# Performance work log

Measured on AMD Instinct MI355X. Metric: run time of the kernel, lower is better.

Reference implementation:

```python
import jax, jax.numpy as jnp
import numpy as np

T, H, I, E, K = 4096, 1024, 2048, 32, 4


def setup_inputs() -> dict:
    key = jax.random.key(0)
    ks = jax.random.split(key, 8)
    s = lambda k, shape, std: (jax.random.normal(k, shape, jnp.float32) * std)
    return {
        "x": s(ks[0], (T, H), 1.0),
        "router_w": s(ks[1], (E, H), 0.02),
        "gate_w": s(ks[2], (E, H, I), 0.02),
        "up_w": s(ks[3], (E, H, I), 0.02),
        "down_w": s(ks[4], (E, I, H), 0.02),
        "shared_gate_w": s(ks[5], (H, I), 0.02),
        "shared_up_w": s(ks[6], (H, I), 0.02),
        "shared_down_w": s(ks[7], (I, H), 0.02),
        "top_k": K,
    }


def _moe_forward(x, router_w, gate_w, up_w, down_w, sg, su, sd, top_k):
    # x: [T, H]; expert weights: gate/up [E, H, I], down [E, I, H]
    Tn = x.shape[0]
    En = router_w.shape[0]

    # Router: softmax over experts, top-k selection, renormalize selected probs
    logits = x @ router_w.T                                   # [T, E]
    probs = jax.nn.softmax(logits, axis=-1)
    topk_p, topk_i = jax.lax.top_k(probs, top_k)              # [T, K]
    topk_p = topk_p / jnp.sum(topk_p, axis=-1, keepdims=True)

    # Dense combine weights: combine[t, e] = routing weight of expert e for token t
    combine = jnp.zeros((Tn, En), x.dtype).at[
        jnp.arange(Tn)[:, None], topk_i].add(topk_p)          # [T, E]

    def expert_step(acc, inp):
        wg, wu, wd, c = inp                                   # [H,I], [H,I], [I,H], [T]
        h = jax.nn.silu(x @ wg) * (x @ wu)                    # [T, I] SwiGLU
        return acc + c[:, None] * (h @ wd), None

    acc0 = jnp.zeros_like(x)
    out, _ = jax.lax.scan(expert_step, acc0,
                          (gate_w, up_w, down_w, combine.T))

    # Shared expert: always applied
    shared = (jax.nn.silu(x @ sg) * (x @ su)) @ sd            # [T, H]
    return out + shared


def reference(x, router_w, gate_w, up_w, down_w,
              shared_gate_w, shared_up_w, shared_down_w, top_k):
    return _moe_forward(x, router_w, gate_w, up_w, down_w,
                        shared_gate_w, shared_up_w, shared_down_w, top_k)
```

## Files before the change

kernel.cpp:

```cpp
#include <hip/hip_runtime.h>
#include <hip/hip_bf16.h>

#define T_TOK 4096
#define H_DIM 1024
#define I_DIM 2048
#define N_EXP 32
#define TOPK  4
#define TKTOT (T_TOK * TOPK)
#define ROWS_MAX 24576
#define MAX_TILES 192
#define BM 128
#define BK 64
#define LDB 72

typedef _Float16 f16;
typedef __attribute__((ext_vector_type(2))) f16  f16x2;
typedef __attribute__((ext_vector_type(4))) f16  f16x4;
typedef __attribute__((ext_vector_type(8))) f16  f16x8;
typedef __attribute__((ext_vector_type(4))) float f32x4;

__device__ __forceinline__ void glds16(const f16* g, f16* l) {
  __builtin_amdgcn_global_load_lds(
      (const __attribute__((address_space(1))) void*)g,
      (__attribute__((address_space(3))) void*)l, 16, 0, 0);
}
__device__ __forceinline__ void sfence() { __builtin_amdgcn_sched_barrier(0); }
__device__ __forceinline__ void bar_vm36() {
  sfence();
  asm volatile("s_waitcnt vmcnt(36) lgkmcnt(0)" ::: "memory");
  sfence();
  __builtin_amdgcn_s_barrier();
  sfence();
}
__device__ __forceinline__ void bar_vm20() {
  sfence();
  asm volatile("s_waitcnt vmcnt(20) lgkmcnt(0)" ::: "memory");
  sfence();
  __builtin_amdgcn_s_barrier();
  sfence();
}
__device__ __forceinline__ void bar_vm12() {
  sfence();
  asm volatile("s_waitcnt vmcnt(12) lgkmcnt(0)" ::: "memory");
  sfence();
  __builtin_amdgcn_s_barrier();
  sfence();
}
__device__ __forceinline__ void bar_vm0() {
  sfence();
  asm volatile("s_waitcnt vmcnt(0) lgkmcnt(0)" ::: "memory");
  sfence();
  __builtin_amdgcn_s_barrier();
  sfence();
}
__device__ __forceinline__ void bar_post() {
  sfence();
  __builtin_amdgcn_s_barrier();
  sfence();
}

__global__ void prep_kernel(const float* __restrict__ x, f16* __restrict__ xb,
                            int* __restrict__ row_token,
                            int* __restrict__ counts) {
  int gid = blockIdx.x * blockDim.x + threadIdx.x;
  float4 v = *(const float4*)(x + (size_t)gid * 4);
  f16x4 hv = { (f16)v.x, (f16)v.y, (f16)v.z, (f16)v.w };
  *(f16x4*)(xb + (size_t)gid * 4) = hv;
  if (gid < ROWS_MAX) row_token[gid] = (gid < T_TOK) ? gid : 0;
  if (gid < N_EXP) counts[gid] = 0;
}

__global__ void router_kernel(const float* __restrict__ x,
                              const float* __restrict__ rw,
                              int* __restrict__ expert_sel,
                              float* __restrict__ weight_sel,
                              int* __restrict__ counts) {
  int wid = threadIdx.x >> 6, lane = threadIdx.x & 63;
  int t = blockIdx.x * 4 + wid;
  float xr[16];
#pragma unroll
  for (int j = 0; j < 16; ++j) xr[j] = x[(size_t)t * H_DIM + lane + j * 64];
  float l[32];
#pragma unroll
  for (int e = 0; e < 32; ++e) {
    float p = 0.f;
#pragma unroll
    for (int j = 0; j < 16; ++j) p += xr[j] * rw[(size_t)e * H_DIM + lane + j * 64];
#pragma unroll
    for (int off = 32; off; off >>= 1) p += __shfl_xor(p, off, 64);
    l[e] = p;
  }
  if (lane == 0) {
    unsigned used = 0;
    int sel[4]; float lv[4];
#pragma unroll
    for (int k = 0; k < 4; ++k) {
      float bv = -3.4e38f; int bi = 0;
#pragma unroll
      for (int e = 0; e < 32; ++e) {
        bool better = (((used >> e) & 1u) == 0u) && (l[e] > bv);
        bv = better ? l[e] : bv;
        bi = better ? e : bi;
      }
      used |= 1u << bi; sel[k] = bi; lv[k] = bv;
    }
    float m = lv[0];
    float p0 = __expf(lv[0] - m), p1 = __expf(lv[1] - m);
    float p2 = __expf(lv[2] - m), p3 = __expf(lv[3] - m);
    float s = p0 + p1 + p2 + p3;
    float wv[4] = { p0 / s, p1 / s, p2 / s, p3 / s };
#pragma unroll
    for (int k = 0; k < 4; ++k) {
      expert_sel[t * 4 + k] = sel[k];
      weight_sel[t * 4 + k] = wv[k];
      atomicAdd(&counts[sel[k]], 1);
    }
  }
}

__global__ void scan_kernel(const int* __restrict__ counts, int* __restrict__ cursor,
                            int* __restrict__ tile_expert, int* __restrict__ tile_row0,
                            int* __restrict__ ntiles) {
  if (threadIdx.x != 0 || blockIdx.x != 0) return;
  int nt = 0;
  for (int i = 0; i < T_TOK / BM; ++i) { tile_expert[nt] = N_EXP; tile_row0[nt] = i * BM; ++nt; }
  int pos = T_TOK;
  for (int e = 0; e < N_EXP; ++e) {
    cursor[e] = pos;
    int c = counts[e];
    int nte = (c + BM - 1) / BM;
    for (int i = 0; i < nte; ++i) { tile_expert[nt] = e; tile_row0[nt] = pos + i * BM; ++nt; }
    pos += nte * BM;
  }
  ntiles[0] = nt;
}

__global__ void scatter_kernel(const int* __restrict__ expert_sel,
                               int* __restrict__ cursor,
                               int* __restrict__ row_token,
                               int* __restrict__ slot_of) {
  int i = blockIdx.x * blockDim.x + threadIdx.x;
  if (i >= TKTOT) return;
  int e = expert_sel[i];
  int pos = atomicAdd(&cursor[e], 1);
  row_token[pos] = i >> 2;
  slot_of[i] = pos;
}

struct Bf2 { float2 g[8]; };
__device__ __forceinline__ Bf2 fetch_b2(const float* __restrict__ src, size_t ldn) {
  Bf2 r;
#pragma unroll
  for (int j = 0; j < 8; ++j) r.g[j] = *(const float2*)(src + (size_t)j * ldn);
  return r;
}
__device__ __forceinline__ void write_b2(const Bf2& b,
                                         f16 (*__restrict__ Bs)[LDB], int nq, int kr) {
  const float* ga = (const float*)b.g;
  int ks = (8 * kr) ^ ((nq & 7) << 3);
#pragma unroll
  for (int i = 0; i < 2; ++i) {
    union { f16x2 p[4]; f16x8 v; } u;
#pragma unroll
    for (int j = 0; j < 4; ++j)
      u.p[j] = __builtin_bit_cast(
          f16x2, __builtin_amdgcn_cvt_pkrtz(ga[(2 * j) * 2 + i],
                                            ga[(2 * j + 1) * 2 + i]));
    *(f16x8*)&Bs[2 * nq + i][ks] = u.v;
  }
}
__device__ __forceinline__ int rswz1(int row, int kf16) {
  return kf16 ^ (((row >> 1) & 7) << 3);
}

struct Bf4 { float4 g[8]; };
__device__ __forceinline__ Bf4 fetch_b4(const float* __restrict__ src, size_t ldn) {
  Bf4 r;
#pragma unroll
  for (int j = 0; j < 8; ++j) r.g[j] = *(const float4*)(src + (size_t)j * ldn);
  return r;
}
__device__ __forceinline__ void write_b4(const Bf4& b,
                                         f16 (*__restrict__ Bs)[LDB], int nq, int kr) {
  const float* ga = (const float*)b.g;
  int ks = (8 * kr) ^ ((nq & 7) << 3);
#pragma unroll
  for (int i = 0; i < 4; ++i) {
    union { f16x2 p[4]; f16x8 v; } u;
#pragma unroll
    for (int j = 0; j < 4; ++j)
      u.p[j] = __builtin_bit_cast(
          f16x2, __builtin_amdgcn_cvt_pkrtz(ga[(2 * j) * 4 + i],
                                            ga[(2 * j + 1) * 4 + i]));
    *(f16x8*)&Bs[4 * nq + i][ks] = u.v;
  }
}
__device__ __forceinline__ int rswz2(int row, int kf16) {
  return kf16 ^ (((row >> 2) & 7) << 3);
}

__global__ __launch_bounds__(256, 2) void gemm1_kernel(
    const f16* __restrict__ xb,
    const float* __restrict__ gate_w, const float* __restrict__ up_w,
    const float* __restrict__ sgw, const float* __restrict__ suw,
    const int* __restrict__ row_token,
    const int* __restrict__ tile_expert, const int* __restrict__ tile_row0,
    const int* __restrict__ ntiles, f16* __restrict__ hbuf) {
  int d = blockIdx.y * gridDim.x + blockIdx.x;
  int l = (d & 7) * 768 + (d >> 3);
  int bx = l % MAX_TILES;
  int n0 = (l / MAX_TILES) * 64;
  if (bx >= ntiles[0]) return;
  int e = tile_expert[bx];
  int row0 = tile_row0[bx];
  const float* wg = (e < N_EXP) ? gate_w + (size_t)e * H_DIM * I_DIM : sgw;
  const float* wu = (e < N_EXP) ? up_w   + (size_t)e * H_DIM * I_DIM : suw;

  __shared__ __align__(16) f16 smem[2 * BM * BK + 2 * 64 * LDB];
  f16* A0 = smem;
  f16* A1 = smem + BM * BK;
  f16 (*Bg)[LDB] = (f16(*)[LDB])(smem + 2 * BM * BK);
  f16 (*Bu)[LDB] = (f16(*)[LDB])(smem + 2 * BM * BK + 64 * LDB);
  f16 (*Ct)[LDB] = (f16(*)[LDB])smem;

  int tid = threadIdx.x;
  int lane = tid & 63, wid = tid >> 6;
  int wm = wid >> 1, wn = wid & 1;
  int lr = lane & 15, lk = (lane >> 4) * 8;
  int nq = tid & 31, kr = tid >> 5;

  const f16* abase[4];
#pragma unroll
  for (int it = 0; it < 4; ++it) {
    int idx = tid + it * 256;
    int arow = idx >> 3;
    int atok = row_token[row0 + arow];
    abase[it] = xb + (size_t)atok * H_DIM + ((((idx & 7)) ^ (arow & 7)) << 3);
  }
  const float* wgp = wg + (size_t)(8 * kr) * I_DIM + n0 + 2 * nq;
  const float* wup = wu + (size_t)(8 * kr) * I_DIM + n0 + 2 * nq;

  f32x4 accg[4][2], accu[4][2];
#pragma unroll
  for (int m = 0; m < 4; ++m)
#pragma unroll
    for (int n = 0; n < 2; ++n) { accg[m][n] = (f32x4)0.f; accu[m][n] = (f32x4)0.f; }

  const int NK = H_DIM / BK;

  sfence();
#pragma unroll
  for (int it = 0; it < 4; ++it)
    glds16(abase[it], A0 + (tid + it * 256) * 8);
  sfence();
  Bf2 g0 = fetch_b2(wgp, I_DIM);
  Bf2 u0 = fetch_b2(wup, I_DIM);
  sfence();
  Bf2 g1 = fetch_b2(wgp + (size_t)BK * I_DIM, I_DIM);
  Bf2 u1 = fetch_b2(wup + (size_t)BK * I_DIM, I_DIM);
  sfence();

#define G1_MFMA(ASRC)                                                        \
  {                                                                          \
    const f16* As_ = (ASRC);                                                 \
    __builtin_amdgcn_s_setprio(1);                                           \
    _Pragma("unroll")                                                        \
    for (int kk = 0; kk < BK; kk += 32) {                                    \
      f16x8 a[4], bg[2], bu[2];                                              \
      _Pragma("unroll")                                                      \
      for (int m = 0; m < 4; ++m) {                                          \
        int ar = wm * 64 + m * 16 + lr;                                      \
        int ko = (kk + lk) ^ ((ar & 7) << 3);                                \
        a[m] = *(const f16x8*)(As_ + ar * BK + ko);                          \
      }                                                                      \
      _Pragma("unroll")                                                      \
      for (int n = 0; n < 2; ++n) {                                          \
        int rowb = wn * 32 + n * 16 + lr;                                    \
        int ko = rswz1(rowb, kk + lk);                                       \
        bg[n] = *(const f16x8*)&Bg[rowb][ko];                                \
        bu[n] = *(const f16x8*)&Bu[rowb][ko];                                \
      }                                                                      \
      _Pragma("unroll")                                                      \
      for (int m = 0; m < 4; ++m)                                            \
        _Pragma("unroll")                                                    \
        for (int n = 0; n < 2; ++n) {                                        \
          accg[m][n] = __builtin_amdgcn_mfma_f32_16x16x32_f16(a[m], bg[n], accg[m][n], 0, 0, 0); \
          accu[m][n] = __builtin_amdgcn_mfma_f32_16x16x32_f16(a[m], bu[n], accu[m][n], 0, 0, 0); \
        }                                                                    \
    }                                                                        \
    __builtin_amdgcn_s_setprio(0);                                           \
  }

  for (int ks = 0; ks < NK - 2; ks += 2) {
    {
      write_b2(g0, Bg, nq, kr);
      write_b2(u0, Bu, nq, kr);
      sfence();
#pragma unroll
      for (int it = 0; it < 4; ++it)
        glds16(abase[it] + (ks + 1) * BK, A1 + (tid + it * 256) * 8);
      sfence();
      g0 = fetch_b2(wgp + (size_t)(ks + 2) * BK * I_DIM, I_DIM);
      u0 = fetch_b2(wup + (size_t)(ks + 2) * BK * I_DIM, I_DIM);
      sfence();
      bar_vm36();
      G1_MFMA(A0);
      bar_post();
    }
    {
      write_b2(g1, Bg, nq, kr);
      write_b2(u1, Bu, nq, kr);
      sfence();
#pragma unroll
      for (int it = 0; it < 4; ++it)
        glds16(abase[it] + (ks + 2) * BK, A0 + (tid + it * 256) * 8);
      sfence();
      g1 = fetch_b2(wgp + (size_t)(ks + 3) * BK * I_DIM, I_DIM);
      u1 = fetch_b2(wup + (size_t)(ks + 3) * BK * I_DIM, I_DIM);
      sfence();
      bar_vm36();
      G1_MFMA(A1);
      bar_post();
    }
  }
  {
    write_b2(g0, Bg, nq, kr);
    write_b2(u0, Bu, nq, kr);
    sfence();
#pragma unroll
    for (int it = 0; it < 4; ++it)
      glds16(abase[it] + (NK - 1) * BK, A1 + (tid + it * 256) * 8);
    sfence();
    bar_vm20();
    G1_MFMA(A0);
    bar_post();
  }
  {
    write_b2(g1, Bg, nq, kr);
    write_b2(u1, Bu, nq, kr);
    bar_vm0();
    G1_MFMA(A1);
  }
#undef G1_MFMA

  __syncthreads();
#pragma unroll
  for (int m = 0; m < 4; ++m)
#pragma unroll
    for (int n = 0; n < 2; ++n)
#pragma unroll
      for (int j = 0; j < 4; ++j) {
        float g = accg[m][n][j], u = accu[m][n][j];
        float hv = g / (1.f + __expf(-g)) * u;
        Ct[wm * 64 + m * 16 + (lane >> 4) * 4 + j][wn * 32 + n * 16 + lr] = (f16)hv;
      }
  __syncthreads();
#pragma unroll
  for (int it = 0; it < 4; ++it) {
    int idx = tid + it * 256;
    int r = idx >> 3, g8 = (idx & 7) * 8;
    *(f16x8*)(hbuf + (size_t)(row0 + r) * I_DIM + n0 + g8) = *(const f16x8*)&Ct[r][g8];
  }
}

__global__ __launch_bounds__(256, 2) void gemm2_kernel(
    const f16* __restrict__ hbuf,
    const float* __restrict__ down_w, const float* __restrict__ sdw,
    const int* __restrict__ tile_expert, const int* __restrict__ tile_row0,
    const int* __restrict__ ntiles, f16* __restrict__ ybuf) {
  int d = blockIdx.y * gridDim.x + blockIdx.x;
  int l = (d & 7) * 192 + (d >> 3);
  int bx = l % MAX_TILES;
  int n0 = (l / MAX_TILES) * 128;
  if (bx >= ntiles[0]) return;
  int e = tile_expert[bx];
  int row0 = tile_row0[bx];
  const float* wd = (e < N_EXP) ? down_w + (size_t)e * I_DIM * H_DIM : sdw;

  __shared__ __align__(16) f16 smem[2 * BM * BK + 128 * LDB];
  f16* A0 = smem;
  f16* A1 = smem + BM * BK;
  f16 (*Bd)[LDB] = (f16(*)[LDB])(smem + 2 * BM * BK);
  f16 (*Ct)[136] = (f16(*)[136])smem;

  int tid = threadIdx.x;
  int lane = tid & 63, wid = tid >> 6;
  int wm = wid >> 1, wn = wid & 1;
  int lr = lane & 15, lk = (lane >> 4) * 8;
  int nq = tid & 31, kr = tid >> 5;

  const f16* abase[4];
#pragma unroll
  for (int it = 0; it < 4; ++it) {
    int idx = tid + it * 256;
    int arow = idx >> 3;
    abase[it] = hbuf + (size_t)(row0 + arow) * I_DIM + ((((idx & 7)) ^ (arow & 7)) << 3);
  }
  const float* wdp = wd + (size_t)(8 * kr) * H_DIM + n0 + 4 * nq;

  f32x4 acc[4][4];
#pragma unroll
  for (int m = 0; m < 4; ++m)
#pragma unroll
    for (int n = 0; n < 4; ++n) acc[m][n] = (f32x4)0.f;

  const int NK = I_DIM / BK;

  sfence();
#pragma unroll
  for (int it = 0; it < 4; ++it)
    glds16(abase[it], A0 + (tid + it * 256) * 8);
  sfence();
  Bf4 d0 = fetch_b4(wdp, H_DIM);
  sfence();
  Bf4 d1 = fetch_b4(wdp + (size_t)BK * H_DIM, H_DIM);
  sfence();

#define G2_MFMA(ASRC)                                                        \
  {                                                                          \
    const f16* As_ = (ASRC);                                                 \
    __builtin_amdgcn_s_setprio(1);                                           \
    _Pragma("unroll")                                                        \
    for (int kk = 0; kk < BK; kk += 32) {                                    \
      f16x8 a[4], bd[4];                                                     \
      _Pragma("unroll")                                                      \
      for (int m = 0; m < 4; ++m) {                                          \
        int ar = wm * 64 + m * 16 + lr;                                      \
        int ko = (kk + lk) ^ ((ar & 7) << 3);                                \
        a[m] = *(const f16x8*)(As_ + ar * BK + ko);                          \
      }                                                                      \
      _Pragma("unroll")                                                      \
      for (int n = 0; n < 4; ++n) {                                          \
        int rowb = wn * 64 + n * 16 + lr;                                    \
        bd[n] = *(const f16x8*)&Bd[rowb][rswz2(rowb, kk + lk)];              \
      }                                                                      \
      _Pragma("unroll")                                                      \
      for (int m = 0; m < 4; ++m)                                            \
        _Pragma("unroll")                                                    \
        for (int n = 0; n < 4; ++n)                                          \
          acc[m][n] = __builtin_amdgcn_mfma_f32_16x16x32_f16(a[m], bd[n], acc[m][n], 0, 0, 0); \
    }                                                                        \
    __builtin_amdgcn_s_setprio(0);                                           \
  }

  for (int ks = 0; ks < NK - 2; ks += 2) {
    {
      write_b4(d0, Bd, nq, kr);
      sfence();
#pragma unroll
      for (int it = 0; it < 4; ++it)
        glds16(abase[it] + (ks + 1) * BK, A1 + (tid + it * 256) * 8);
      sfence();
      d0 = fetch_b4(wdp + (size_t)(ks + 2) * BK * H_DIM, H_DIM);
      sfence();
      bar_vm20();
      G2_MFMA(A0);
      bar_post();
    }
    {
      write_b4(d1, Bd, nq, kr);
      sfence();
#pragma unroll
      for (int it = 0; it < 4; ++it)
        glds16(abase[it] + (ks + 2) * BK, A0 + (tid + it * 256) * 8);
      sfence();
      d1 = fetch_b4(wdp + (size_t)(ks + 3) * BK * H_DIM, H_DIM);
      sfence();
      bar_vm20();
      G2_MFMA(A1);
      bar_post();
    }
  }
  {
    write_b4(d0, Bd, nq, kr);
    sfence();
#pragma unroll
    for (int it = 0; it < 4; ++it)
      glds16(abase[it] + (NK - 1) * BK, A1 + (tid + it * 256) * 8);
    sfence();
    bar_vm12();
    G2_MFMA(A0);
    bar_post();
  }
  {
    write_b4(d1, Bd, nq, kr);
    bar_vm0();
    G2_MFMA(A1);
  }
#undef G2_MFMA

  __syncthreads();
#pragma unroll
  for (int m = 0; m < 4; ++m)
#pragma unroll
    for (int n = 0; n < 4; ++n)
#pragma unroll
      for (int j = 0; j < 4; ++j)
        Ct[wm * 64 + m * 16 + (lane >> 4) * 4 + j][wn * 64 + n * 16 + lr] =
            (f16)acc[m][n][j];
  __syncthreads();
#pragma unroll
  for (int it = 0; it < 8; ++it) {
    int idx = tid + it * 256;
    int r = idx >> 4, g8 = (idx & 15) * 8;
    *(f16x8*)(ybuf + (size_t)(row0 + r) * H_DIM + n0 + g8) = *(const f16x8*)&Ct[r][g8];
  }
}

__global__ void gather_kernel(const f16* __restrict__ ybuf,
                              const int* __restrict__ slot_of,
                              const float* __restrict__ weight_sel,
                              float* __restrict__ out) {
  int gid = blockIdx.x * blockDim.x + threadIdx.x;
  int t = gid >> 7, s8 = (gid & 127) * 8;
  f16x8 ysh = *(const f16x8*)(ybuf + (size_t)t * H_DIM + s8);
  float a[8];
#pragma unroll
  for (int j = 0; j < 8; ++j) a[j] = (float)ysh[j];
#pragma unroll
  for (int k = 0; k < 4; ++k) {
    int sl = slot_of[t * 4 + k];
    float w = weight_sel[t * 4 + k];
    f16x8 v = *(const f16x8*)(ybuf + (size_t)sl * H_DIM + s8);
#pragma unroll
    for (int j = 0; j < 8; ++j) a[j] += w * (float)v[j];
  }
  float4 o0 = { a[0], a[1], a[2], a[3] };
  float4 o1 = { a[4], a[5], a[6], a[7] };
  *(float4*)(out + (size_t)t * H_DIM + s8) = o0;
  *(float4*)(out + (size_t)t * H_DIM + s8 + 4) = o1;
}

extern "C" void kernel_launch(void* const* d_in, const int* in_sizes, int n_in,
                              void* d_out, int out_size, void* d_ws, size_t ws_size,
                              hipStream_t stream) {
  const float* x        = (const float*)d_in[0];
  const float* router_w = (const float*)d_in[1];
  const float* gate_w   = (const float*)d_in[2];
  const float* up_w     = (const float*)d_in[3];
  const float* down_w   = (const float*)d_in[4];
  const float* sgw      = (const float*)d_in[5];
  const float* suw      = (const float*)d_in[6];
  const float* sdw      = (const float*)d_in[7];
  float* out = (float*)d_out;

  char* w = (char*)d_ws;
  f16*   xb         = (f16*)w;   w += (size_t)T_TOK * H_DIM * 2;
  int*   expert_sel = (int*)w;   w += (size_t)TKTOT * 4;
  float* weight_sel = (float*)w; w += (size_t)TKTOT * 4;
  int*   slot_of    = (int*)w;   w += (size_t)TKTOT * 4;
  int*   counts     = (int*)w;   w += 256;
  int*   cursor     = (int*)w;   w += 256;
  int*   tile_exp   = (int*)w;   w += MAX_TILES * 4;
  int*   tile_row0  = (int*)w;   w += MAX_TILES * 4;
  int*   ntiles     = (int*)w;   w += 256;
  int*   row_token  = (int*)w;   w += (size_t)ROWS_MAX * 4;
  f16*   hbuf       = (f16*)w;   w += (size_t)ROWS_MAX * I_DIM * 2;
  f16*   ybuf       = (f16*)w;   w += (size_t)ROWS_MAX * H_DIM * 2;
  if ((size_t)(w - (char*)d_ws) > ws_size) return;

  prep_kernel<<<(T_TOK * H_DIM / 4) / 256, 256, 0, stream>>>(x, xb, row_token, counts);
  router_kernel<<<T_TOK / 4, 256, 0, stream>>>(x, router_w, expert_sel, weight_sel, counts);
  scan_kernel<<<1, 64, 0, stream>>>(counts, cursor, tile_exp, tile_row0, ntiles);
  scatter_kernel<<<TKTOT / 256, 256, 0, stream>>>(expert_sel, cursor, row_token, slot_of);
  gemm1_kernel<<<dim3(MAX_TILES, I_DIM / 64), 256, 0, stream>>>(
      xb, gate_w, up_w, sgw, suw, row_token, tile_exp, tile_row0, ntiles, hbuf);
  gemm2_kernel<<<dim3(MAX_TILES, H_DIM / 128), 256, 0, stream>>>(
      hbuf, down_w, sdw, tile_exp, tile_row0, ntiles, ybuf);
  gather_kernel<<<(T_TOK * (H_DIM / 8)) / 256, 256, 0, stream>>>(
      ybuf, slot_of, weight_sel, out);
}
```

Baseline: 678.7 us.

## Split gate/up GEMMs across 8-warp blocks, double-buffer B tiles, parallelize tile scan

Both grouped GEMM kernels now launch 512 threads per block instead of 256. In gemm1, warps 0-3 compute the gate projection and warps 4-7 the up projection, and SiLU and the product are applied in the epilogue through shared memory. gemm2 spreads its 128-column tile over 8 warps, and both kernels double-buffer the B tile in LDS with adjusted vmcnt waits. The tile-building scan becomes a wavefront shuffle prefix sum instead of a single-thread loop. This lowers per-thread register and accumulator pressure and adds latency hiding, at the cost of doubled B staging LDS and an f16 rounding step before the gate*up multiply.

After: 676.1 us. No clear change (-0.4%).

```diff
diff --git a/kernel.cpp b/kernel.cpp
--- a/kernel.cpp
+++ b/kernel.cpp
@@ -25,23 +25,16 @@
       (__attribute__((address_space(3))) void*)l, 16, 0, 0);
 }
 __device__ __forceinline__ void sfence() { __builtin_amdgcn_sched_barrier(0); }
-__device__ __forceinline__ void bar_vm36() {
-  sfence();
-  asm volatile("s_waitcnt vmcnt(36) lgkmcnt(0)" ::: "memory");
+__device__ __forceinline__ void bar_vm18() {
+  sfence();
+  asm volatile("s_waitcnt vmcnt(18) lgkmcnt(0)" ::: "memory");
   sfence();
   __builtin_amdgcn_s_barrier();
   sfence();
 }
-__device__ __forceinline__ void bar_vm20() {
-  sfence();
-  asm volatile("s_waitcnt vmcnt(20) lgkmcnt(0)" ::: "memory");
-  sfence();
-  __builtin_amdgcn_s_barrier();
-  sfence();
-}
-__device__ __forceinline__ void bar_vm12() {
-  sfence();
-  asm volatile("s_waitcnt vmcnt(12) lgkmcnt(0)" ::: "memory");
+__device__ __forceinline__ void bar_vm10() {
+  sfence();
+  asm volatile("s_waitcnt vmcnt(10) lgkmcnt(0)" ::: "memory");
   sfence();
   __builtin_amdgcn_s_barrier();
   sfence();
@@ -121,18 +114,32 @@
 __global__ void scan_kernel(const int* __restrict__ counts, int* __restrict__ cursor,
                             int* __restrict__ tile_expert, int* __restrict__ tile_row0,
                             int* __restrict__ ntiles) {
-  if (threadIdx.x != 0 || blockIdx.x != 0) return;
-  int nt = 0;
-  for (int i = 0; i < T_TOK / BM; ++i) { tile_expert[nt] = N_EXP; tile_row0[nt] = i * BM; ++nt; }
-  int pos = T_TOK;
-  for (int e = 0; e < N_EXP; ++e) {
-    cursor[e] = pos;
-    int c = counts[e];
-    int nte = (c + BM - 1) / BM;
-    for (int i = 0; i < nte; ++i) { tile_expert[nt] = e; tile_row0[nt] = pos + i * BM; ++nt; }
-    pos += nte * BM;
-  }
-  ntiles[0] = nt;
+  int lane = threadIdx.x;
+  if (lane < T_TOK / BM) { tile_expert[lane] = N_EXP; tile_row0[lane] = lane * BM; }
+  int nte = 0, rows = 0;
+  if (lane < N_EXP) {
+    int c = counts[lane];
+    nte = (c + BM - 1) / BM;
+    rows = nte * BM;
+  }
+  int pnte = nte, prows = rows;
+#pragma unroll
+  for (int off = 1; off < 64; off <<= 1) {
+    int t1 = __shfl_up(pnte, off, 64);
+    int t2 = __shfl_up(prows, off, 64);
+    if (lane >= off) { pnte += t1; prows += t2; }
+  }
+  int excl_nte = pnte - nte, excl_rows = prows - rows;
+  if (lane < N_EXP) {
+    int pos = T_TOK + excl_rows;
+    cursor[lane] = pos;
+    int tb = T_TOK / BM + excl_nte;
+    for (int i = 0; i < nte; ++i) {
+      tile_expert[tb + i] = lane;
+      tile_row0[tb + i] = pos + i * BM;
+    }
+    if (lane == N_EXP - 1) ntiles[0] = tb + nte;
+  }
 }
 
 __global__ void scatter_kernel(const int* __restrict__ expert_sel,
@@ -154,8 +161,8 @@
   for (int j = 0; j < 8; ++j) r.g[j] = *(const float2*)(src + (size_t)j * ldn);
   return r;
 }
-__device__ __forceinline__ void write_b2(const Bf2& b,
-                                         f16 (*__restrict__ Bs)[LDB], int nq, int kr) {
+__device__ __forceinline__ void write_b2(const Bf2& b, f16* __restrict__ Bs,
+                                         int nq, int kr) {
   const float* ga = (const float*)b.g;
   int ks = (8 * kr) ^ ((nq & 7) << 3);
 #pragma unroll
@@ -166,40 +173,14 @@
       u.p[j] = __builtin_bit_cast(
           f16x2, __builtin_amdgcn_cvt_pkrtz(ga[(2 * j) * 2 + i],
                                             ga[(2 * j + 1) * 2 + i]));
-    *(f16x8*)&Bs[2 * nq + i][ks] = u.v;
+    *(f16x8*)(Bs + (2 * nq + i) * LDB + ks) = u.v;
   }
 }
 __device__ __forceinline__ int rswz1(int row, int kf16) {
   return kf16 ^ (((row >> 1) & 7) << 3);
 }
 
-struct Bf4 { float4 g[8]; };
-__device__ __forceinline__ Bf4 fetch_b4(const float* __restrict__ src, size_t ldn) {
-  Bf4 r;
-#pragma unroll
-  for (int j = 0; j < 8; ++j) r.g[j] = *(const float4*)(src + (size_t)j * ldn);
-  return r;
-}
-__device__ __forceinline__ void write_b4(const Bf4& b,
-                                         f16 (*__restrict__ Bs)[LDB], int nq, int kr) {
-  const float* ga = (const float*)b.g;
-  int ks = (8 * kr) ^ ((nq & 7) << 3);
-#pragma unroll
-  for (int i = 0; i < 4; ++i) {
-    union { f16x2 p[4]; f16x8 v; } u;
-#pragma unroll
-    for (int j = 0; j < 4; ++j)
-      u.p[j] = __builtin_bit_cast(
-          f16x2, __builtin_amdgcn_cvt_pkrtz(ga[(2 * j) * 4 + i],
-                                            ga[(2 * j + 1) * 4 + i]));
-    *(f16x8*)&Bs[4 * nq + i][ks] = u.v;
-  }
-}
-__device__ __forceinline__ int rswz2(int row, int kf16) {
-  return kf16 ^ (((row >> 2) & 7) << 3);
-}
-
-__global__ __launch_bounds__(256, 2) void gemm1_kernel(
+__global__ __launch_bounds__(512, 2) void gemm1_kernel(
     const f16* __restrict__ xb,
     const float* __restrict__ gate_w, const float* __restrict__ up_w,
     const float* __restrict__ sgw, const float* __restrict__ suw,
@@ -216,57 +197,59 @@
   const float* wg = (e < N_EXP) ? gate_w + (size_t)e * H_DIM * I_DIM : sgw;
   const float* wu = (e < N_EXP) ? up_w   + (size_t)e * H_DIM * I_DIM : suw;
 
-  __shared__ __align__(16) f16 smem[2 * BM * BK + 2 * 64 * LDB];
+  __shared__ __align__(16) f16 smem[2 * BM * BK + 2 * 2 * 64 * LDB];
   f16* A0 = smem;
   f16* A1 = smem + BM * BK;
-  f16 (*Bg)[LDB] = (f16(*)[LDB])(smem + 2 * BM * BK);
-  f16 (*Bu)[LDB] = (f16(*)[LDB])(smem + 2 * BM * BK + 64 * LDB);
-  f16 (*Ct)[LDB] = (f16(*)[LDB])smem;
+  f16* Bbase = smem + 2 * BM * BK;
+  f16* Ctg = Bbase;
+  f16* Ctu = Bbase + 9216;
 
   int tid = threadIdx.x;
   int lane = tid & 63, wid = tid >> 6;
-  int wm = wid >> 1, wn = wid & 1;
+  int mat = wid >> 2;
+  int w4 = wid & 3;
+  int wm = w4 >> 1, wn = w4 & 1;
   int lr = lane & 15, lk = (lane >> 4) * 8;
-  int nq = tid & 31, kr = tid >> 5;
-
-  const f16* abase[4];
-#pragma unroll
-  for (int it = 0; it < 4; ++it) {
-    int idx = tid + it * 256;
-    int arow = idx >> 3;
-    int atok = row_token[row0 + arow];
-    abase[it] = xb + (size_t)atok * H_DIM + ((((idx & 7)) ^ (arow & 7)) << 3);
-  }
-  const float* wgp = wg + (size_t)(8 * kr) * I_DIM + n0 + 2 * nq;
-  const float* wup = wu + (size_t)(8 * kr) * I_DIM + n0 + 2 * nq;
-
-  f32x4 accg[4][2], accu[4][2];
+
+  int t8 = tid & 255;
+  int nq = t8 & 31, kr = t8 >> 5;
+  const float* wsrc = (mat ? wu : wg) + (size_t)(8 * kr) * I_DIM + n0 + 2 * nq;
+
+  const f16* abase0;
+  const f16* abase1;
+  {
+    int idx = tid;
+    int arow = idx >> 3, sl = idx & 7;
+    abase0 = xb + (size_t)row_token[row0 + arow] * H_DIM + ((sl ^ (arow & 7)) << 3);
+    idx = tid + 512;
+    arow = idx >> 3; sl = idx & 7;
+    abase1 = xb + (size_t)row_token[row0 + arow] * H_DIM + ((sl ^ (arow & 7)) << 3);
+  }
+
+  f32x4 acc[4][2];
 #pragma unroll
   for (int m = 0; m < 4; ++m)
 #pragma unroll
-    for (int n = 0; n < 2; ++n) { accg[m][n] = (f32x4)0.f; accu[m][n] = (f32x4)0.f; }
+    for (int n = 0; n < 2; ++n) acc[m][n] = (f32x4)0.f;
 
   const int NK = H_DIM / BK;
 
-  sfence();
-#pragma unroll
-  for (int it = 0; it < 4; ++it)
-    glds16(abase[it], A0 + (tid + it * 256) * 8);
-  sfence();
-  Bf2 g0 = fetch_b2(wgp, I_DIM);
-  Bf2 u0 = fetch_b2(wup, I_DIM);
-  sfence();
-  Bf2 g1 = fetch_b2(wgp + (size_t)BK * I_DIM, I_DIM);
-  Bf2 u1 = fetch_b2(wup + (size_t)BK * I_DIM, I_DIM);
-  sfence();
-
-#define G1_MFMA(ASRC)                                                        \
+  Bf2 pb0 = fetch_b2(wsrc, I_DIM);
+  sfence();
+  glds16(abase0, A0 + tid * 8);
+  glds16(abase1, A0 + (tid + 512) * 8);
+  sfence();
+  Bf2 pb1 = fetch_b2(wsrc + (size_t)BK * I_DIM, I_DIM);
+  sfence();
+
+#define G1_MFMA(ASRC, BSRC)                                                  \
   {                                                                          \
     const f16* As_ = (ASRC);                                                 \
+    const f16* Bs_ = (BSRC);                                                 \
     __builtin_amdgcn_s_setprio(1);                                           \
     _Pragma("unroll")                                                        \
     for (int kk = 0; kk < BK; kk += 32) {                                    \
-      f16x8 a[4], bg[2], bu[2];                                              \
+      f16x8 a[4], b[2];                                                      \
       _Pragma("unroll")                                                      \
       for (int m = 0; m < 4; ++m) {                                          \
         int ar = wm * 64 + m * 16 + lr;                                      \
@@ -276,94 +259,90 @@
       _Pragma("unroll")                                                      \
       for (int n = 0; n < 2; ++n) {                                          \
         int rowb = wn * 32 + n * 16 + lr;                                    \
-        int ko = rswz1(rowb, kk + lk);                                       \
-        bg[n] = *(const f16x8*)&Bg[rowb][ko];                                \
-        bu[n] = *(const f16x8*)&Bu[rowb][ko];                                \
+        b[n] = *(const f16x8*)(Bs_ + rowb * LDB + rswz1(rowb, kk + lk));     \
       }                                                                      \
       _Pragma("unroll")                                                      \
       for (int m = 0; m < 4; ++m)                                            \
         _Pragma("unroll")                                                    \
-        for (int n = 0; n < 2; ++n) {                                        \
-          accg[m][n] = __builtin_amdgcn_mfma_f32_16x16x32_f16(a[m], bg[n], accg[m][n], 0, 0, 0); \
-          accu[m][n] = __builtin_amdgcn_mfma_f32_16x16x32_f16(a[m], bu[n], accu[m][n], 0, 0, 0); \
-        }                                                                    \
+        for (int n = 0; n < 2; ++n)                                          \
+          acc[m][n] = __builtin_amdgcn_mfma_f32_16x16x32_f16(a[m], b[n], acc[m][n], 0, 0, 0); \
     }                                                                        \
     __builtin_amdgcn_s_setprio(0);                                           \
   }
 
   for (int ks = 0; ks < NK - 2; ks += 2) {
     {
-      write_b2(g0, Bg, nq, kr);
-      write_b2(u0, Bu, nq, kr);
-      sfence();
-#pragma unroll
-      for (int it = 0; it < 4; ++it)
-        glds16(abase[it] + (ks + 1) * BK, A1 + (tid + it * 256) * 8);
-      sfence();
-      g0 = fetch_b2(wgp + (size_t)(ks + 2) * BK * I_DIM, I_DIM);
-      u0 = fetch_b2(wup + (size_t)(ks + 2) * BK * I_DIM, I_DIM);
-      sfence();
-      bar_vm36();
-      G1_MFMA(A0);
+      write_b2(pb0, Bbase + 0 * 9216 + mat * 4608, nq, kr);
+      sfence();
+      glds16(abase0 + (ks + 1) * BK, A1 + tid * 8);
+      glds16(abase1 + (ks + 1) * BK, A1 + (tid + 512) * 8);
+      sfence();
+      pb0 = fetch_b2(wsrc + (size_t)(ks + 2) * BK * I_DIM, I_DIM);
+      sfence();
+      bar_vm18();
+      G1_MFMA(A0, Bbase + 0 * 9216 + mat * 4608);
       bar_post();
     }
     {
-      write_b2(g1, Bg, nq, kr);
-      write_b2(u1, Bu, nq, kr);
-      sfence();
-#pragma unroll
-      for (int it = 0; it < 4; ++it)
-        glds16(abase[it] + (ks + 2) * BK, A0 + (tid + it * 256) * 8);
-      sfence();
-      g1 = fetch_b2(wgp + (size_t)(ks + 3) * BK * I_DIM, I_DIM);
-      u1 = fetch_b2(wup + (size_t)(ks + 3) * BK * I_DIM, I_DIM);
-      sfence();
-      bar_vm36();
-      G1_MFMA(A1);
+      write_b2(pb1, Bbase + 1 * 9216 + mat * 4608, nq, kr);
+      sfence();
+      glds16(abase0 + (ks + 2) * BK, A0 + tid * 8);
+      glds16(abase1 + (ks + 2) * BK, A0 + (tid + 512) * 8);
+      sfence();
+      pb1 = fetch_b2(wsrc + (size_t)(ks + 3) * BK * I_DIM, I_DIM);
+      sfence();
+      bar_vm18();
+      G1_MFMA(A1, Bbase + 1 * 9216 + mat * 4608);
       bar_post();
     }
   }
   {
-    write_b2(g0, Bg, nq, kr);
-    write_b2(u0, Bu, nq, kr);
+    write_b2(pb0, Bbase + 0 * 9216 + mat * 4608, nq, kr);
     sfence();
-#pragma unroll
-    for (int it = 0; it < 4; ++it)
-      glds16(abase[it] + (NK - 1) * BK, A1 + (tid + it * 256) * 8);
+    glds16(abase0 + (NK - 1) * BK, A1 + tid * 8);
+    glds16(abase1 + (NK - 1) * BK, A1 + (tid + 512) * 8);
     sfence();
-    bar_vm20();
-    G1_MFMA(A0);
+    bar_vm10();
+    G1_MFMA(A0, Bbase + 0 * 9216 + mat * 4608);
     bar_post();
   }
   {
-    write_b2(g1, Bg, nq, kr);
-    write_b2(u1, Bu, nq, kr);
+    write_b2(pb1, Bbase + 1 * 9216 + mat * 4608, nq, kr);
     bar_vm0();
-    G1_MFMA(A1);
+    G1_MFMA(A1, Bbase + 1 * 9216 + mat * 4608);
   }
 #undef G1_MFMA
 
   __syncthreads();
-#pragma unroll
-  for (int m = 0; m < 4; ++m)
-#pragma unroll
-    for (int n = 0; n < 2; ++n)
-#pragma unroll
-      for (int j = 0; j < 4; ++j) {
-        float g = accg[m][n][j], u = accu[m][n][j];
-        float hv = g / (1.f + __expf(-g)) * u;
-        Ct[wm * 64 + m * 16 + (lane >> 4) * 4 + j][wn * 32 + n * 16 + lr] = (f16)hv;
-      }
+  {
+    f16* ct = mat ? Ctu : Ctg;
+#pragma unroll
+    for (int m = 0; m < 4; ++m)
+#pragma unroll
+      for (int n = 0; n < 2; ++n)
+#pragma unroll
+        for (int j = 0; j < 4; ++j) {
+          float v = acc[m][n][j];
+          if (mat == 0) v = v / (1.f + __expf(-v));
+          ct[(wm * 64 + m * 16 + (lane >> 4) * 4 + j) * LDB +
+             wn * 32 + n * 16 + lr] = (f16)v;
+        }
+  }
   __syncthreads();
 #pragma unroll
-  for (int it = 0; it < 4; ++it) {
-    int idx = tid + it * 256;
+  for (int it = 0; it < 2; ++it) {
+    int idx = tid + it * 512;
     int r = idx >> 3, g8 = (idx & 7) * 8;
-    *(f16x8*)(hbuf + (size_t)(row0 + r) * I_DIM + n0 + g8) = *(const f16x8*)&Ct[r][g8];
-  }
-}
-
-__global__ __launch_bounds__(256, 2) void gemm2_kernel(
+    f16x8 g = *(const f16x8*)(Ctg + r * LDB + g8);
+    f16x8 u = *(const f16x8*)(Ctu + r * LDB + g8);
+    f16x8 h;
+#pragma unroll
+    for (int j = 0; j < 8; ++j) h[j] = g[j] * u[j];
+    *(f16x8*)(hbuf + (size_t)(row0 + r) * I_DIM + n0 + g8) = h;
+  }
+}
+
+__global__ __launch_bounds__(512, 2) void gemm2_kernel(
     const f16* __restrict__ hbuf,
     const float* __restrict__ down_w, const float* __restrict__ sdw,
     const int* __restrict__ tile_expert, const int* __restrict__ tile_row0,
@@ -377,52 +356,55 @@
   int row0 = tile_row0[bx];
   const float* wd = (e < N_EXP) ? down_w + (size_t)e * I_DIM * H_DIM : sdw;
 
-  __shared__ __align__(16) f16 smem[2 * BM * BK + 128 * LDB];
+  __shared__ __align__(16) f16 smem[2 * BM * BK + 2 * 128 * LDB];
   f16* A0 = smem;
   f16* A1 = smem + BM * BK;
-  f16 (*Bd)[LDB] = (f16(*)[LDB])(smem + 2 * BM * BK);
-  f16 (*Ct)[136] = (f16(*)[136])smem;
+  f16* Bbase = smem + 2 * BM * BK;
+  f16 (*Ct)[136] = (f16(*)[136])Bbase;
 
   int tid = threadIdx.x;
   int lane = tid & 63, wid = tid >> 6;
-  int wm = wid >> 1, wn = wid & 1;
+  int wm = wid >> 2, wn = wid & 3;
   int lr = lane & 15, lk = (lane >> 4) * 8;
-  int nq = tid & 31, kr = tid >> 5;
-
-  const f16* abase[4];
-#pragma unroll
-  for (int it = 0; it < 4; ++it) {
-    int idx = tid + it * 256;
-    int arow = idx >> 3;
-    abase[it] = hbuf + (size_t)(row0 + arow) * I_DIM + ((((idx & 7)) ^ (arow & 7)) << 3);
-  }
-  const float* wdp = wd + (size_t)(8 * kr) * H_DIM + n0 + 4 * nq;
-
-  f32x4 acc[4][4];
+
+  int nq = tid & 63, kr = tid >> 6;
+  const float* wsrc = wd + (size_t)(8 * kr) * H_DIM + n0 + 2 * nq;
+
+  const f16* abase0;
+  const f16* abase1;
+  {
+    int idx = tid;
+    int arow = idx >> 3, sl = idx & 7;
+    abase0 = hbuf + (size_t)(row0 + arow) * I_DIM + ((sl ^ (arow & 7)) << 3);
+    idx = tid + 512;
+    arow = idx >> 3; sl = idx & 7;
+    abase1 = hbuf + (size_t)(row0 + arow) * I_DIM + ((sl ^ (arow & 7)) << 3);
+  }
+
+  f32x4 acc[4][2];
 #pragma unroll
   for (int m = 0; m < 4; ++m)
 #pragma unroll
-    for (int n = 0; n < 4; ++n) acc[m][n] = (f32x4)0.f;
+    for (int n = 0; n < 2; ++n) acc[m][n] = (f32x4)0.f;
 
   const int NK = I_DIM / BK;
 
-  sfence();
-#pragma unroll
-  for (int it = 0; it < 4; ++it)
-    glds16(abase[it], A0 + (tid + it * 256) * 8);
-  sfence();
-  Bf4 d0 = fetch_b4(wdp, H_DIM);
-  sfence();
-  Bf4 d1 = fetch_b4(wdp + (size_t)BK * H_DIM, H_DIM);
-  sfence();
-
-#define G2_MFMA(ASRC)                                                        \
+  Bf2 pb0 = fetch_b2(wsrc, H_DIM);
+  sfence();
+  glds16(abase0, A0 + tid * 8);
+  glds16(abase1, A0 + (tid + 512) * 8);
+  sfence();
+  Bf2 pb1 = fetch_b2(wsrc + (size_t)BK * H_DIM, H_DIM);
+  sfence();
+
+#define G2_MFMA(ASRC, BSRC)                                                  \
   {                                                                          \
     const f16* As_ = (ASRC);                                                 \
+    const f16* Bs_ = (BSRC);                                                 \
     __builtin_amdgcn_s_setprio(1);                                           \
     _Pragma("unroll")                                                        \
     for (int kk = 0; kk < BK; kk += 32) {                                    \
-      f16x8 a[4], bd[4];                                                     \
+      f16x8 a[4], b[2];                                                      \
       _Pragma("unroll")                                                      \
       for (int m = 0; m < 4; ++m) {                                          \
         int ar = wm * 64 + m * 16 + lr;                                      \
@@ -430,62 +412,59 @@
         a[m] = *(const f16x8*)(As_ + ar * BK + ko);                          \
       }                                                                      \
       _Pragma("unroll")                                                      \
-      for (int n = 0; n < 4; ++n) {                                          \
-        int rowb = wn * 64 + n * 16 + lr;                                    \
-        bd[n] = *(const f16x8*)&Bd[rowb][rswz2(rowb, kk + lk)];              \
+      for (int n = 0; n < 2; ++n) {                                          \
+        int rowb = wn * 32 + n * 16 + lr;                                    \
+        b[n] = *(const f16x8*)(Bs_ + rowb * LDB + rswz1(rowb, kk + lk));     \
       }                                                                      \
       _Pragma("unroll")                                                      \
       for (int m = 0; m < 4; ++m)                                            \
         _Pragma("unroll")                                                    \
-        for (int n = 0; n < 4; ++n)                                          \
-          acc[m][n] = __builtin_amdgcn_mfma_f32_16x16x32_f16(a[m], bd[n], acc[m][n], 0, 0, 0); \
+        for (int n = 0; n < 2; ++n)                                          \
+          acc[m][n] = __builtin_amdgcn_mfma_f32_16x16x32_f16(a[m], b[n], acc[m][n], 0, 0, 0); \
     }                                                                        \
     __builtin_amdgcn_s_setprio(0);                                           \
   }
 
   for (int ks = 0; ks < NK - 2; ks += 2) {
     {
-      write_b4(d0, Bd, nq, kr);
-      sfence();
-#pragma unroll
-      for (int it = 0; it < 4; ++it)
-        glds16(abase[it] + (ks + 1) * BK, A1 + (tid + it * 256) * 8);
-      sfence();
-      d0 = fetch_b4(wdp + (size_t)(ks + 2) * BK * H_DIM, H_DIM);
-      sfence();
-      bar_vm20();
-      G2_MFMA(A0);
+      write_b2(pb0, Bbase + 0 * 9216, nq, kr);
+      sfence();
+      glds16(abase0 + (ks + 1) * BK, A1 + tid * 8);
+      glds16(abase1 + (ks + 1) * BK, A1 + (tid + 512) * 8);
+      sfence();
+      pb0 = fetch_b2(wsrc + (size_t)(ks + 2) * BK * H_DIM, H_DIM);
+      sfence();
+      bar_vm18();
+      G2_MFMA(A0, Bbase + 0 * 9216);
       bar_post();
     }
     {
-      write_b4(d1, Bd, nq, kr);
-      sfence();
-#pragma unroll
-      for (int it = 0; it < 4; ++it)
-        glds16(abase[it] + (ks + 2) * BK, A0 + (tid + it * 256) * 8);
-      sfence();
-      d1 = fetch_b4(wdp + (size_t)(ks + 3) * BK * H_DIM, H_DIM);
-      sfence();
-      bar_vm20();
-      G2_MFMA(A1);
+      write_b2(pb1, Bbase + 1 * 9216, nq, kr);
+      sfence();
+      glds16(abase0 + (ks + 2) * BK, A0 + tid * 8);
+      glds16(abase1 + (ks + 2) * BK, A0 + (tid + 512) * 8);
+      sfence();
+      pb1 = fetch_b2(wsrc + (size_t)(ks + 3) * BK * H_DIM, H_DIM);
+      sfence();
+      bar_vm18();
+      G2_MFMA(A1, Bbase + 1 * 9216);
       bar_post();
     }
   }
   {
-    write_b4(d0, Bd, nq, kr);
+    write_b2(pb0, Bbase + 0 * 9216, nq, kr);
     sfence();
-#pragma unroll
-    for (int it = 0; it < 4; ++it)
-      glds16(abase[it] + (NK - 1) * BK, A1 + (tid + it * 256) * 8);
+    glds16(abase0 + (NK - 1) * BK, A1 + tid * 8);
+    glds16(abase1 + (NK - 1) * BK, A1 + (tid + 512) * 8);
     sfence();
-    bar_vm12();
-    G2_MFMA(A0);
+    bar_vm10();
+    G2_MFMA(A0, Bbase + 0 * 9216);
     bar_post();
   }
   {
-    write_b4(d1, Bd, nq, kr);
+    write_b2(pb1, Bbase + 1 * 9216, nq, kr);
     bar_vm0();
-    G2_MFMA(A1);
+    G2_MFMA(A1, Bbase + 1 * 9216);
   }
 #undef G2_MFMA
 
@@ -493,15 +472,15 @@
 #pragma unroll
   for (int m = 0; m < 4; ++m)
 #pragma unroll
-    for (int n = 0; n < 4; ++n)
+    for (int n = 0; n < 2; ++n)
 #pragma unroll
       for (int j = 0; j < 4; ++j)
-        Ct[wm * 64 + m * 16 + (lane >> 4) * 4 + j][wn * 64 + n * 16 + lr] =
+        Ct[wm * 64 + m * 16 + (lane >> 4) * 4 + j][wn * 32 + n * 16 + lr] =
             (f16)acc[m][n][j];
   __syncthreads();
 #pragma unroll
-  for (int it = 0; it < 8; ++it) {
-    int idx = tid + it * 256;
+  for (int it = 0; it < 4; ++it) {
+    int idx = tid + it * 512;
     int r = idx >> 4, g8 = (idx & 15) * 8;
     *(f16x8*)(ybuf + (size_t)(row0 + r) * H_DIM + n0 + g8) = *(const f16x8*)&Ct[r][g8];
   }
@@ -563,9 +542,9 @@
   router_kernel<<<T_TOK / 4, 256, 0, stream>>>(x, router_w, expert_sel, weight_sel, counts);
   scan_kernel<<<1, 64, 0, stream>>>(counts, cursor, tile_exp, tile_row0, ntiles);
   scatter_kernel<<<TKTOT / 256, 256, 0, stream>>>(expert_sel, cursor, row_token, slot_of);
-  gemm1_kernel<<<dim3(MAX_TILES, I_DIM / 64), 256, 0, stream>>>(
+  gemm1_kernel<<<dim3(MAX_TILES, I_DIM / 64), 512, 0, stream>>>(
       xb, gate_w, up_w, sgw, suw, row_token, tile_exp, tile_row0, ntiles, hbuf);
-  gemm2_kernel<<<dim3(MAX_TILES, H_DIM / 128), 256, 0, stream>>>(
+  gemm2_kernel<<<dim3(MAX_TILES, H_DIM / 128), 512, 0, stream>>>(
       hbuf, down_w, sdw, tile_exp, tile_row0, ntiles, ybuf);
   gather_kernel<<<(T_TOK * (H_DIM / 8)) / 256, 256, 0, stream>>>(
       ybuf, slot_of, weight_sel, out);
```
